# Performance work log

Measured on AMD Instinct MI355X. Metric: run time of the kernel, lower is better.

The kernel has to match this reference:

```python
import jax, jax.numpy as jnp
import numpy as np

B, F, V, D, K = 16384, 39, 30000, 16, 20
EPS = 1e-5


def bn_eval(x, g, b):
    # inference-mode BatchNorm1d with running_mean=0, running_var=1
    return g * x / jnp.sqrt(1.0 + EPS) + b


def setup_inputs() -> dict:
    key = jax.random.key(0)
    ks = jax.random.split(key, 12)
    x = jax.random.randint(ks[0], (B, F), 0, V)
    emb_table = jax.random.normal(ks[1], (F * V, D), dtype=jnp.float32) * 0.05
    w_c = jax.random.normal(ks[2], (F, F * D), dtype=jnp.float32) * 0.05
    w0 = jax.random.normal(ks[3], (1024, F * D), dtype=jnp.float32) * 0.04
    w1 = jax.random.normal(ks[4], (512, 1024), dtype=jnp.float32) * 0.03
    w_out = jax.random.normal(ks[5], (1, 512), dtype=jnp.float32) * 0.04
    return {
        'x': x, 'emb_table': emb_table,
        'w_c': w_c, 'b_c': jnp.zeros((F,)), 'g_c': jnp.ones((F,)), 'be_c': jnp.zeros((F,)),
        'w0': w0, 'b0': jnp.zeros((1024,)), 'g0': jnp.ones((1024,)), 'be0': jnp.zeros((1024,)),
        'w1': w1, 'b1': jnp.zeros((512,)), 'g1': jnp.ones((512,)), 'be1': jnp.zeros((512,)),
        'w_out': w_out, 'b_out': jnp.zeros((1,)),
    }


def reference(x, emb_table, w_c, b_c, g_c, be_c, w0, b0, g0, be0,
              w1, b1, g1, be1, w_out, b_out):
    offsets = jnp.arange(F, dtype=x.dtype) * V          # per-field offsets
    idx = x + offsets[None, :]                          # [B, F]
    emb = emb_table[idx]                                # [B, F, D] gather

    # controller_mlp: flatten (batch, D, F) layout like torch transpose(1,2)
    flat = jnp.transpose(emb, (0, 2, 1)).reshape(B, F * D)
    h = jax.nn.relu(bn_eval(flat @ w_c.T + b_c, g_c, be_c))
    scores = jax.nn.softmax(h, axis=1)                  # [B, F]

    # kmax_pooling: top-k field indices, sorted ascending, gather weights
    _, kidx = jax.lax.top_k(scores, K)
    kidx = jnp.sort(kidx, axis=1)                       # [B, K]
    w = jnp.take_along_axis(scores, kidx, axis=1)       # [B, K]

    # forward_select: gather selected field embeddings, weight them
    sel = jnp.take_along_axis(emb, kidx[:, :, None], axis=1)  # [B, K, D]
    weighted = sel * w[:, :, None]

    # scatter back into full field slots (unselected fields are zero)
    full = jnp.zeros((B, F, D), weighted.dtype)
    bidx = jnp.arange(B)[:, None]
    full = full.at[bidx, kidx].set(weighted)            # [B, F, D]

    z = jnp.transpose(full, (0, 2, 1)).reshape(B, F * D)
    z = jax.nn.relu(bn_eval(z @ w0.T + b0, g0, be0))
    z = jax.nn.relu(bn_eval(z @ w1.T + b1, g1, be1))
    out = jax.nn.sigmoid(z @ w_out.T + b_out)           # [B, 1]
    return out.squeeze(-1)
```

## Files before the change

### kernel.cpp

```cpp
#include <hip/hip_runtime.h>
#include <math.h>

#define B_SZ 16384
#define F_N 39
#define V_N 30000
#define D_N 16
#define K_SEL 20
#define FD 624
#define KP0 640
#define NCP 48
#define N0 1024
#define N1 512
#define CBR 16
#define ALD 648

typedef unsigned short u16;
typedef __attribute__((ext_vector_type(8))) short bf16x8;
typedef __attribute__((ext_vector_type(8))) unsigned short u16x8;
typedef __attribute__((ext_vector_type(4))) float f32x4;

__device__ __forceinline__ float bf2f(u16 v) {
    union { unsigned u; float f; } x; x.u = ((unsigned)v) << 16;
    return x.f;
}
__device__ __forceinline__ unsigned cvtpk2(float a, float b) {
    unsigned d;
    asm("v_cvt_pk_bf16_f32 %0, %1, %2" : "=v"(d) : "v"(a), "v"(b));
    return d;
}

#define GLD16(gp, lp) __builtin_amdgcn_global_load_lds( \
    (const __attribute__((address_space(1))) unsigned int*)(gp), \
    (__attribute__((address_space(3))) unsigned int*)(lp), 16, 0, 0)

#define MFMA16(a, b, c) __builtin_amdgcn_mfma_f32_16x16x32_bf16((a), (b), (c), 0, 0, 0)

__global__ __launch_bounds__(256) void prep_all_kernel(
    const float* __restrict__ w0, const float* __restrict__ w1,
    const float* __restrict__ w_c, const float* __restrict__ b_c,
    const float* __restrict__ g_c, const float* __restrict__ be_c,
    u16* __restrict__ w0b, u16* __restrict__ w1b, u16* __restrict__ wcb,
    float* __restrict__ bcp, float* __restrict__ gcp, float* __restrict__ becp)
{
    __shared__ float Lb[8][624];
    const int bid = blockIdx.x;
    const int t   = threadIdx.x;

    if (bid < 134) {
        const bool is_w0 = (bid < 128);
        const int r0 = is_w0 ? bid * 8 : (bid - 128) * 8;
        const int nrows_src = is_w0 ? N0 : F_N;
        const float* __restrict__ src = is_w0 ? w0 : w_c;
        u16* __restrict__ dst = is_w0 ? w0b : wcb;

        for (int j = t; j < 8 * 156; j += 256) {
            const int row = j / 156;
            const int c4  = j - row * 156;
            const int n   = r0 + row;
            if (n < nrows_src)
                *(float4*)&Lb[row][c4 * 4] =
                    *(const float4*)&src[(size_t)n * FD + c4 * 4];
        }
        __syncthreads();

        for (int j = t; j < 8 * 320; j += 256) {
            const int row = j / 320;
            const int pr  = j - row * 320;
            const int n   = r0 + row;
            const int k0  = pr * 2;
            float v0 = 0.f, v1 = 0.f;
            if (n < nrows_src) {
                const int d0 = k0 & 15,       f0 = k0 >> 4;
                const int d1 = (k0 + 1) & 15, f1 = (k0 + 1) >> 4;
                if (f0 < F_N) v0 = Lb[row][d0 * F_N + f0];
                if (f1 < F_N) v1 = Lb[row][d1 * F_N + f1];
            }
            *(unsigned*)&dst[(size_t)n * KP0 + k0] = cvtpk2(v0, v1);
        }
        return;
    }
    if (bid < 390) {
        const size_t e0 = (size_t)(bid - 134) * 2048 + t * 8;
        float4 v0 = *(const float4*)(w1 + e0);
        float4 v1 = *(const float4*)(w1 + e0 + 4);
        uint4 o = { cvtpk2(v0.x, v0.y), cvtpk2(v0.z, v0.w),
                    cvtpk2(v1.x, v1.y), cvtpk2(v1.z, v1.w) };
        *(uint4*)(w1b + e0) = o;
        return;
    }
    if (t < 3 * NCP) {
        const int which = t / NCP, n = t - which * NCP;
        float v = 0.f;
        if (n < F_N) v = (which == 0) ? b_c[n] : (which == 1) ? g_c[n] : be_c[n];
        ((which == 0) ? bcp : (which == 1) ? gcp : becp)[n] = v;
    }
}

__global__ __launch_bounds__(256) void fused_controller_kernel(
    const int* __restrict__ x, const float* __restrict__ emb_table,
    const u16* __restrict__ wcb, const float* __restrict__ bcp,
    const float* __restrict__ gcp, const float* __restrict__ becp,
    u16* __restrict__ zb)
{
    __shared__ __align__(16) u16 Al[CBR * ALD];
    __shared__ float vv[CBR][49];
    __shared__ f32x4 part[4][64][3];
    __shared__ float selw[CBR][F_N];

    const int t    = threadIdx.x;
    const int wave = t >> 6;
    const int lane = t & 63;
    const int b0   = blockIdx.x * CBR;

    {
        const int p0 = t, p1 = t + 256, p2 = t + 512;
        const int xi0 = x[b0 * F_N + p0];
        const int xi1 = x[b0 * F_N + p1];
        const int xi2 = (p2 < CBR * F_N) ? x[b0 * F_N + p2] : 0;
        const int pp[3] = { p0, p1, p2 };
        const int xx[3] = { xi0, xi1, xi2 };
        #pragma unroll
        for (int s = 0; s < 3; ++s) {
            const int p = pp[s];
            if (p < CBR * F_N) {
                const int row = p / F_N;
                const int f   = p - row * F_N;
                const float4* src =
                    (const float4*)(emb_table + (size_t)(xx[s] + f * V_N) * D_N);
                float4 v0 = src[0], v1 = src[1], v2 = src[2], v3 = src[3];
                uint4 o0 = { cvtpk2(v0.x, v0.y), cvtpk2(v0.z, v0.w),
                             cvtpk2(v1.x, v1.y), cvtpk2(v1.z, v1.w) };
                uint4 o1 = { cvtpk2(v2.x, v2.y), cvtpk2(v2.z, v2.w),
                             cvtpk2(v3.x, v3.y), cvtpk2(v3.z, v3.w) };
                *(uint4*)&Al[row * ALD + f * D_N]     = o0;
                *(uint4*)&Al[row * ALD + f * D_N + 8] = o1;
            }
        }
    }
    __syncthreads();

    const int m = lane & 15;
    const int q = lane >> 4;
    f32x4 acc0 = {}, acc1 = {}, acc2 = {};
    {
        const u16* ap  = &Al[m * ALD + wave * 160 + q * 8];
        const u16* bp0 = wcb + (size_t)(0  + m) * KP0 + wave * 160 + q * 8;
        const u16* bp1 = wcb + (size_t)(16 + m) * KP0 + wave * 160 + q * 8;
        const u16* bp2 = wcb + (size_t)(32 + m) * KP0 + wave * 160 + q * 8;
        #pragma unroll
        for (int k = 0; k < 5; ++k) {
            bf16x8 af = *(const bf16x8*)ap;
            bf16x8 b0r = *(const bf16x8*)bp0;
            bf16x8 b1r = *(const bf16x8*)bp1;
            bf16x8 b2r = *(const bf16x8*)bp2;
            acc0 = MFMA16(af, b0r, acc0);
            acc1 = MFMA16(af, b1r, acc1);
            acc2 = MFMA16(af, b2r, acc2);
            ap += 32; bp0 += 32; bp1 += 32; bp2 += 32;
        }
    }
    part[wave][lane][0] = acc0;
    part[wave][lane][1] = acc1;
    part[wave][lane][2] = acc2;
    __syncthreads();

    {
        f32x4 r0 = part[0][lane][0] + part[1][lane][0] + part[2][lane][0] + part[3][lane][0];
        f32x4 r1 = part[0][lane][1] + part[1][lane][1] + part[2][lane][1] + part[3][lane][1];
        f32x4 r2 = part[0][lane][2] + part[1][lane][2] + part[2][lane][2] + part[3][lane][2];

        const float rs = rsqrtf(1.0f + 1e-5f);
        if (q == wave) {
            #pragma unroll
            for (int j = 0; j < 3; ++j) {
                const f32x4 a = (j == 0) ? r0 : (j == 1) ? r1 : r2;
                const int n = j * 16 + m;
                const float gn = gcp[n] * rs;
                const float bn = becp[n];
                const float bi = bcp[n];
                #pragma unroll
                for (int r = 0; r < 4; ++r)
                    vv[wave * 4 + r][n] = fmaxf(fmaf(gn, a[r] + bi, bn), 0.f);
            }
        }
    }
    __syncthreads();

    {
        const int row = wave * 4 + (lane >> 4);
        const int fl  = lane & 15;
        float e[3] = {0.f, 0.f, 0.f};
        float mloc = -1e30f;
        #pragma unroll
        for (int it = 0; it < 3; ++it) {
            const int f = fl + 16 * it;
            if (f < F_N) { e[it] = vv[row][f]; mloc = fmaxf(mloc, e[it]); }
        }
        mloc = fmaxf(mloc, __shfl_xor(mloc, 1, 64));
        mloc = fmaxf(mloc, __shfl_xor(mloc, 2, 64));
        mloc = fmaxf(mloc, __shfl_xor(mloc, 4, 64));
        mloc = fmaxf(mloc, __shfl_xor(mloc, 8, 64));
        float sloc = 0.f;
        #pragma unroll
        for (int it = 0; it < 3; ++it) {
            const int f = fl + 16 * it;
            if (f < F_N) { e[it] = expf(e[it] - mloc); sloc += e[it]; }
        }
        sloc += __shfl_xor(sloc, 1, 64);
        sloc += __shfl_xor(sloc, 2, 64);
        sloc += __shfl_xor(sloc, 4, 64);
        sloc += __shfl_xor(sloc, 8, 64);
        const float inv = 1.f / sloc;
        #pragma unroll
        for (int it = 0; it < 3; ++it) {
            const int f = fl + 16 * it;
            if (f < F_N) vv[row][f] = e[it];
        }

        int rank[3] = {};
        for (int gg = 0; gg < F_N; ++gg) {
            const float o = vv[row][gg];
            #pragma unroll
            for (int it = 0; it < 3; ++it) {
                const int f = fl + 16 * it;
                if (f < F_N)
                    rank[it] += (o > e[it] || (o == e[it] && gg < f)) ? 1 : 0;
            }
        }
        #pragma unroll
        for (int it = 0; it < 3; ++it) {
            const int f = fl + 16 * it;
            if (f < F_N)
                selw[row][f] = (rank[it] < K_SEL) ? e[it] * inv : 0.f;
        }
    }
    __syncthreads();

    for (int gp = t; gp < CBR * 40; gp += 256) {
        const int row  = gp / 40;
        const int slot = gp - row * 40;
        u16* dst = zb + (size_t)(b0 + row) * KP0 + slot * D_N;
        uint4 o0 = {0u,0u,0u,0u}, o1 = {0u,0u,0u,0u};
        if (slot < F_N) {
            const float w = selw[row][slot];
            u16x8 a0 = *(u16x8*)&Al[row * ALD + slot * D_N];
            u16x8 a1 = *(u16x8*)&Al[row * ALD + slot * D_N + 8];
            o0 = (uint4){ cvtpk2(bf2f(a0[0]) * w, bf2f(a0[1]) * w),
                          cvtpk2(bf2f(a0[2]) * w, bf2f(a0[3]) * w),
                          cvtpk2(bf2f(a0[4]) * w, bf2f(a0[5]) * w),
                          cvtpk2(bf2f(a0[6]) * w, bf2f(a0[7]) * w) };
            o1 = (uint4){ cvtpk2(bf2f(a1[0]) * w, bf2f(a1[1]) * w),
                          cvtpk2(bf2f(a1[2]) * w, bf2f(a1[3]) * w),
                          cvtpk2(bf2f(a1[4]) * w, bf2f(a1[5]) * w),
                          cvtpk2(bf2f(a1[6]) * w, bf2f(a1[7]) * w) };
        }
        *(uint4*)dst       = o0;
        *(uint4*)(dst + 8) = o1;
    }
}

__global__ __launch_bounds__(512) void fused_mlp_kernel(
    const u16* __restrict__ Azb, const u16* __restrict__ W0,
    const u16* __restrict__ W1,
    const float* __restrict__ b0v, const float* __restrict__ g0v,
    const float* __restrict__ be0v,
    const float* __restrict__ b1v, const float* __restrict__ g1v,
    const float* __restrict__ be1v,
    const float* __restrict__ wov, const float* __restrict__ bov,
    float* __restrict__ out)
{
    __shared__ __align__(16) u16 SM[3 * 16384];
    __shared__ __align__(16) u16 H0[64 * 264];
    __shared__ float red[4][64];

    const int t    = threadIdx.x;
    const int lane = t & 63;
    const int wave = t >> 6;
    const int wm = wave >> 2, wn = wave & 3;
    const int q = lane >> 4, lr16 = lane & 15;
    const int brow = blockIdx.x * 64;

    const int srow = t >> 2;
    const int cC   = (t & 3) ^ ((t >> 3) & 3);
    const int dA  = t * 8;
    const int dB0 = 2048 + t * 8;
    const int dB1 = 2048 + (t + 512) * 8;

    const u16* gAz = Azb + (size_t)(brow + srow) * KP0 + cC * 8;

    int aoffA[2], boffA[4], aoffB[2], boffB[8];
    #pragma unroll
    for (int i = 0; i < 2; ++i) {
        const int ra = wm * 32 + i * 16 + lr16;
        aoffA[i] = ra * 32 + ((q ^ ((ra >> 1) & 3)) * 8);
        aoffB[i] = ra * 264 + q * 8;
    }
    #pragma unroll
    for (int j = 0; j < 4; ++j) {
        const int rb = wn * 64 + j * 16 + lr16;
        boffA[j] = 2048 + rb * 32 + ((q ^ ((rb >> 1) & 3)) * 8);
    }
    #pragma unroll
    for (int j = 0; j < 8; ++j) {
        const int rb = wn * 128 + j * 16 + lr16;
        boffB[j] = rb * 32 + ((q ^ ((rb >> 1) & 3)) * 8);
    }

    f32x4 acc1[2][8] = {};
    const float rs = rsqrtf(1.0f + 1e-5f);

    for (int nt = 0; nt < 4; ++nt) {
        f32x4 acc0[2][4] = {};
        const u16* pA  = gAz;
        const u16* pB0 = W0 + (size_t)(nt * 256 + srow)       * KP0 + cC * 8;
        const u16* pB1 = W0 + (size_t)(nt * 256 + srow + 128) * KP0 + cC * 8;

        if (t < 256) GLD16(pA, SM + dA);
        GLD16(pB0, SM + dB0);
        GLD16(pB1, SM + dB1);
        pA += 32; pB0 += 32; pB1 += 32;
        if (t < 256) GLD16(pA, SM + 16384 + dA);
        GLD16(pB0, SM + 16384 + dB0);
        GLD16(pB1, SM + 16384 + dB1);
        pA += 32; pB0 += 32; pB1 += 32;

        int cur = 0, stg = 2;
        for (int it = 0; it < 19; ++it) {
            if (t < 256) { asm volatile("s_waitcnt vmcnt(3)" ::: "memory"); }
            else         { asm volatile("s_waitcnt vmcnt(2)" ::: "memory"); }
            __builtin_amdgcn_s_barrier();
            __builtin_amdgcn_sched_barrier(0);
            const u16* sc = SM + cur * 16384;
            bf16x8 a0 = *(const bf16x8*)(sc + aoffA[0]);
            bf16x8 a1 = *(const bf16x8*)(sc + aoffA[1]);
            bf16x8 f0 = *(const bf16x8*)(sc + boffA[0]);
            bf16x8 f1 = *(const bf16x8*)(sc + boffA[1]);
            bf16x8 f2 = *(const bf16x8*)(sc + boffA[2]);
            bf16x8 f3 = *(const bf16x8*)(sc + boffA[3]);
            if (it + 2 < 20) {
                u16* ss = SM + stg * 16384;
                if (t < 256) GLD16(pA, ss + dA);
                GLD16(pB0, ss + dB0);
                GLD16(pB1, ss + dB1);
                pA += 32; pB0 += 32; pB1 += 32;
            }
            asm volatile("s_waitcnt lgkmcnt(0)" ::: "memory");
            __builtin_amdgcn_sched_barrier(0);
            __builtin_amdgcn_s_setprio(1);
            acc0[0][0] = MFMA16(a0, f0, acc0[0][0]);
            acc0[0][1] = MFMA16(a0, f1, acc0[0][1]);
            acc0[0][2] = MFMA16(a0, f2, acc0[0][2]);
            acc0[0][3] = MFMA16(a0, f3, acc0[0][3]);
            acc0[1][0] = MFMA16(a1, f0, acc0[1][0]);
            acc0[1][1] = MFMA16(a1, f1, acc0[1][1]);
            acc0[1][2] = MFMA16(a1, f2, acc0[1][2]);
            acc0[1][3] = MFMA16(a1, f3, acc0[1][3]);
            __builtin_amdgcn_s_setprio(0);
            cur = (cur == 2) ? 0 : cur + 1;
            stg = (stg == 2) ? 0 : stg + 1;
        }
        asm volatile("s_waitcnt vmcnt(0)" ::: "memory");
        __builtin_amdgcn_s_barrier();
        __builtin_amdgcn_sched_barrier(0);
        {
            const u16* sc = SM + 16384;
            bf16x8 a0 = *(const bf16x8*)(sc + aoffA[0]);
            bf16x8 a1 = *(const bf16x8*)(sc + aoffA[1]);
            bf16x8 f0 = *(const bf16x8*)(sc + boffA[0]);
            bf16x8 f1 = *(const bf16x8*)(sc + boffA[1]);
            bf16x8 f2 = *(const bf16x8*)(sc + boffA[2]);
            bf16x8 f3 = *(const bf16x8*)(sc + boffA[3]);
            asm volatile("s_waitcnt lgkmcnt(0)" ::: "memory");
            __builtin_amdgcn_sched_barrier(0);
            __builtin_amdgcn_s_setprio(1);
            acc0[0][0] = MFMA16(a0, f0, acc0[0][0]);
            acc0[0][1] = MFMA16(a0, f1, acc0[0][1]);
            acc0[0][2] = MFMA16(a0, f2, acc0[0][2]);
            acc0[0][3] = MFMA16(a0, f3, acc0[0][3]);
            acc0[1][0] = MFMA16(a1, f0, acc0[1][0]);
            acc0[1][1] = MFMA16(a1, f1, acc0[1][1]);
            acc0[1][2] = MFMA16(a1, f2, acc0[1][2]);
            acc0[1][3] = MFMA16(a1, f3, acc0[1][3]);
            __builtin_amdgcn_s_setprio(0);
        }

        const u16* pC = W1 + (size_t)srow * N0 + nt * 256 + cC * 8;
        {
            GLD16(pC,               SM + t * 8);
            GLD16(pC + 131072,      SM + (t + 512) * 8);
            GLD16(pC + 262144,      SM + (t + 1024) * 8);
            GLD16(pC + 393216,      SM + (t + 1536) * 8);
            u16* s2 = SM + 2 * 16384;
            GLD16(pC + 32,          s2 + t * 8);
            GLD16(pC + 131072 + 32, s2 + (t + 512) * 8);
            GLD16(pC + 262144 + 32, s2 + (t + 1024) * 8);
            GLD16(pC + 393216 + 32, s2 + (t + 1536) * 8);
        }

        #pragma unroll
        for (int j = 0; j < 4; ++j) {
            const int n = nt * 256 + wn * 64 + j * 16 + lr16;
            const float gg = g0v[n] * rs;
            const float bb = be0v[n];
            const float bi = b0v[n];
            const int colL = wn * 64 + j * 16 + lr16;
            #pragma unroll
            for (int i = 0; i < 2; ++i) {
                const int mlb = wm * 32 + i * 16 + q * 4;
                float v0 = fmaxf(fmaf(gg, acc0[i][j][0] + bi, bb), 0.f);
                float v1 = fmaxf(fmaf(gg, acc0[i][j][1] + bi, bb), 0.f);
                float v2 = fmaxf(fmaf(gg, acc0[i][j][2] + bi, bb), 0.f);
                float v3 = fmaxf(fmaf(gg, acc0[i][j][3] + bi, bb), 0.f);
                unsigned pa = cvtpk2(v0, v1);
                unsigned pb = cvtpk2(v2, v3);
                H0[(mlb + 0) * 264 + colL] = (u16)pa;
                H0[(mlb + 1) * 264 + colL] = (u16)(pa >> 16);
                H0[(mlb + 2) * 264 + colL] = (u16)pb;
                H0[(mlb + 3) * 264 + colL] = (u16)(pb >> 16);
            }
        }
        asm volatile("s_waitcnt lgkmcnt(0)" ::: "memory");
        __builtin_amdgcn_s_barrier();

        const u16* pCk = pC + 64;
        int cb = 0, sb = 1;
        for (int ks = 0; ks < 7; ++ks) {
            asm volatile("s_waitcnt vmcnt(4)" ::: "memory");
            __builtin_amdgcn_s_barrier();
            __builtin_amdgcn_sched_barrier(0);
            const u16* sc = SM + cb * 16384;
            bf16x8 a0 = *(const bf16x8*)(&H0[aoffB[0] + ks * 32]);
            bf16x8 a1 = *(const bf16x8*)(&H0[aoffB[1] + ks * 32]);
            bf16x8 f0 = *(const bf16x8*)(sc + boffB[0]);
            bf16x8 f1 = *(const bf16x8*)(sc + boffB[1]);
            bf16x8 f2 = *(const bf16x8*)(sc + boffB[2]);
            bf16x8 f3 = *(const bf16x8*)(sc + boffB[3]);
            bf16x8 f4 = *(const bf16x8*)(sc + boffB[4]);
            bf16x8 f5 = *(const bf16x8*)(sc + boffB[5]);
            bf16x8 f6 = *(const bf16x8*)(sc + boffB[6]);
            bf16x8 f7 = *(const bf16x8*)(sc + boffB[7]);
            if (ks + 2 < 8) {
                u16* ss = SM + sb * 16384;
                GLD16(pCk,          ss + t * 8);
                GLD16(pCk + 131072, ss + (t + 512) * 8);
                GLD16(pCk + 262144, ss + (t + 1024) * 8);
                GLD16(pCk + 393216, ss + (t + 1536) * 8);
                pCk += 32;
            }
            asm volatile("s_waitcnt lgkmcnt(0)" ::: "memory");
            __builtin_amdgcn_sched_barrier(0);
            __builtin_amdgcn_s_setprio(1);
            acc1[0][0] = MFMA16(a0, f0, acc1[0][0]);
            acc1[0][1] = MFMA16(a0, f1, acc1[0][1]);
            acc1[0][2] = MFMA16(a0, f2, acc1[0][2]);
            acc1[0][3] = MFMA16(a0, f3, acc1[0][3]);
            acc1[0][4] = MFMA16(a0, f4, acc1[0][4]);
            acc1[0][5] = MFMA16(a0, f5, acc1[0][5]);
            acc1[0][6] = MFMA16(a0, f6, acc1[0][6]);
            acc1[0][7] = MFMA16(a0, f7, acc1[0][7]);
            acc1[1][0] = MFMA16(a1, f0, acc1[1][0]);
            acc1[1][1] = MFMA16(a1, f1, acc1[1][1]);
            acc1[1][2] = MFMA16(a1, f2, acc1[1][2]);
            acc1[1][3] = MFMA16(a1, f3, acc1[1][3]);
            acc1[1][4] = MFMA16(a1, f4, acc1[1][4]);
            acc1[1][5] = MFMA16(a1, f5, acc1[1][5]);
            acc1[1][6] = MFMA16(a1, f6, acc1[1][6]);
            acc1[1][7] = MFMA16(a1, f7, acc1[1][7]);
            __builtin_amdgcn_s_setprio(0);
            cb = (cb == 0) ? 2 : cb - 1;
            sb = (sb == 0) ? 2 : sb - 1;
        }
        asm volatile("s_waitcnt vmcnt(0)" ::: "memory");
        __builtin_amdgcn_s_barrier();
        __builtin_amdgcn_sched_barrier(0);
        {
            const u16* sc = SM + 2 * 16384;
            bf16x8 a0 = *(const bf16x8*)(&H0[aoffB[0] + 7 * 32]);
            bf16x8 a1 = *(const bf16x8*)(&H0[aoffB[1] + 7 * 32]);
            bf16x8 f0 = *(const bf16x8*)(sc + boffB[0]);
            bf16x8 f1 = *(const bf16x8*)(sc + boffB[1]);
            bf16x8 f2 = *(const bf16x8*)(sc + boffB[2]);
            bf16x8 f3 = *(const bf16x8*)(sc + boffB[3]);
            bf16x8 f4 = *(const bf16x8*)(sc + boffB[4]);
            bf16x8 f5 = *(const bf16x8*)(sc + boffB[5]);
            bf16x8 f6 = *(const bf16x8*)(sc + boffB[6]);
            bf16x8 f7 = *(const bf16x8*)(sc + boffB[7]);
            asm volatile("s_waitcnt lgkmcnt(0)" ::: "memory");
            __builtin_amdgcn_sched_barrier(0);
            __builtin_amdgcn_s_setprio(1);
            acc1[0][0] = MFMA16(a0, f0, acc1[0][0]);
            acc1[0][1] = MFMA16(a0, f1, acc1[0][1]);
            acc1[0][2] = MFMA16(a0, f2, acc1[0][2]);
            acc1[0][3] = MFMA16(a0, f3, acc1[0][3]);
            acc1[0][4] = MFMA16(a0, f4, acc1[0][4]);
            acc1[0][5] = MFMA16(a0, f5, acc1[0][5]);
            acc1[0][6] = MFMA16(a0, f6, acc1[0][6]);
            acc1[0][7] = MFMA16(a0, f7, acc1[0][7]);
            acc1[1][0] = MFMA16(a1, f0, acc1[1][0]);
            acc1[1][1] = MFMA16(a1, f1, acc1[1][1]);
            acc1[1][2] = MFMA16(a1, f2, acc1[1][2]);
            acc1[1][3] = MFMA16(a1, f3, acc1[1][3]);
            acc1[1][4] = MFMA16(a1, f4, acc1[1][4]);
            acc1[1][5] = MFMA16(a1, f5, acc1[1][5]);
            acc1[1][6] = MFMA16(a1, f6, acc1[1][6]);
            acc1[1][7] = MFMA16(a1, f7, acc1[1][7]);
            __builtin_amdgcn_s_setprio(0);
        }
    }

    float s[2][4] = {};
    #pragma unroll
    for (int j = 0; j < 8; ++j) {
        const int n1 = wn * 128 + j * 16 + lr16;
        const float wv = wov[n1];
        const float gg = g1v[n1] * rs;
        const float bb = be1v[n1];
        const float bi = b1v[n1];
        #pragma unroll
        for (int i = 0; i < 2; ++i)
            #pragma unroll
            for (int r = 0; r < 4; ++r) {
                float v = fmaxf(fmaf(gg, acc1[i][j][r] + bi, bb), 0.f);
                s[i][r] = fmaf(v, wv, s[i][r]);
            }
    }
    #pragma unroll
    for (int i = 0; i < 2; ++i)
        #pragma unroll
        for (int r = 0; r < 4; ++r) {
            float v = s[i][r];
            v += __shfl_xor(v, 1, 64);
            v += __shfl_xor(v, 2, 64);
            v += __shfl_xor(v, 4, 64);
            v += __shfl_xor(v, 8, 64);
            s[i][r] = v;
        }
    if (lr16 == 0) {
        #pragma unroll
        for (int i = 0; i < 2; ++i)
            #pragma unroll
            for (int r = 0; r < 4; ++r)
                red[wn][wm * 32 + i * 16 + q * 4 + r] = s[i][r];
    }
    __syncthreads();
    if (t < 64) {
        const float v = red[0][t] + red[1][t] + red[2][t] + red[3][t] + bov[0];
        out[brow + t] = 1.f / (1.f + expf(-v));
    }
}

extern "C" void kernel_launch(void* const* d_in, const int* in_sizes, int n_in,
                              void* d_out, int out_size, void* d_ws, size_t ws_size,
                              hipStream_t stream)
{
    const int*   x     = (const int*)  d_in[0];
    const float* emb   = (const float*)d_in[1];
    const float* w_c   = (const float*)d_in[2];
    const float* b_c   = (const float*)d_in[3];
    const float* g_c   = (const float*)d_in[4];
    const float* be_c  = (const float*)d_in[5];
    const float* w0    = (const float*)d_in[6];
    const float* b0    = (const float*)d_in[7];
    const float* g0    = (const float*)d_in[8];
    const float* be0   = (const float*)d_in[9];
    const float* w1    = (const float*)d_in[10];
    const float* b1    = (const float*)d_in[11];
    const float* g1    = (const float*)d_in[12];
    const float* be1   = (const float*)d_in[13];
    const float* w_out = (const float*)d_in[14];
    const float* b_out = (const float*)d_in[15];
    float* out = (float*)d_out;

    u16*   zb    = (u16*)d_ws;
    u16*   w0b   = zb  + (size_t)B_SZ * KP0;
    u16*   w1b   = w0b + (size_t)N0 * KP0;
    u16*   wcb   = w1b + (size_t)N1 * N0;
    float* bcp   = (float*)(wcb + (size_t)NCP * KP0);
    float* gcp   = bcp + NCP;
    float* becp  = gcp + NCP;

    prep_all_kernel<<<391, 256, 0, stream>>>(
        w0, w1, w_c, b_c, g_c, be_c, w0b, w1b, wcb, bcp, gcp, becp);

    fused_controller_kernel<<<B_SZ / CBR, 256, 0, stream>>>(
        x, emb, wcb, bcp, gcp, becp, zb);

    fused_mlp_kernel<<<B_SZ / 64, 512, 0, stream>>>(
        zb, w0b, w1b, b0, g0, be0, b1, g1, be1, w_out, b_out, out);
}
```

Measured before the change: 221.8 us.

## Halve fused MLP row tile to 32 and shrink shared memory for occupancy

The fused MLP kernel now processes 32 batch rows per block instead of 64, doubling the grid to 512 blocks. Shared memory shrinks: stage slots are 9216 elements, the hidden-layer buffer is 32x256 with an XOR swizzle, and the second GEMM is split into two halves of 256 output columns that reuse the same staging slots. The aim is more blocks per CU and better latency hiding on the 256-CU device. The cost is that W0 and W1 are re-streamed twice as often across blocks, and each wave issues fewer MFMAs per LDS load.

```diff
diff --git a/kernel.cpp b/kernel.cpp
--- a/kernel.cpp
+++ b/kernel.cpp
@@ -13,6 +13,7 @@
 #define N1 512
 #define CBR 16
 #define ALD 648
+#define SLOT 9216
 
 typedef unsigned short u16;
 typedef __attribute__((ext_vector_type(8))) short bf16x8;
@@ -269,92 +270,75 @@
     const float* __restrict__ wov, const float* __restrict__ bov,
     float* __restrict__ out)
 {
-    __shared__ __align__(16) u16 SM[3 * 16384];
-    __shared__ __align__(16) u16 H0[64 * 264];
-    __shared__ float red[4][64];
+    __shared__ __align__(16) u16 SM[3 * SLOT + 32 * 256];
+    __shared__ float red[4][32];
 
     const int t    = threadIdx.x;
     const int lane = t & 63;
     const int wave = t >> 6;
     const int wm = wave >> 2, wn = wave & 3;
     const int q = lane >> 4, lr16 = lane & 15;
-    const int brow = blockIdx.x * 64;
-
-    const int srow = t >> 2;
-    const int cC   = (t & 3) ^ ((t >> 3) & 3);
-    const int dA  = t * 8;
-    const int dB0 = 2048 + t * 8;
-    const int dB1 = 2048 + (t + 512) * 8;
-
-    const u16* gAz = Azb + (size_t)(brow + srow) * KP0 + cC * 8;
-
-    int aoffA[2], boffA[4], aoffB[2], boffB[8];
-    #pragma unroll
-    for (int i = 0; i < 2; ++i) {
-        const int ra = wm * 32 + i * 16 + lr16;
-        aoffA[i] = ra * 32 + ((q ^ ((ra >> 1) & 3)) * 8);
-        aoffB[i] = ra * 264 + q * 8;
-    }
+    const int brow = blockIdx.x * 32;
+
+    u16* const H0 = SM + 3 * SLOT;
+
+    const int rS = t >> 2;
+    const int cA = (t & 3) ^ ((rS >> 1) & 3);
+
+    const int raA   = wm * 16 + lr16;
+    const int aoffA = raA * 32 + ((q ^ ((raA >> 1) & 3)) * 8);
+    int boff[4];
     #pragma unroll
     for (int j = 0; j < 4; ++j) {
         const int rb = wn * 64 + j * 16 + lr16;
-        boffA[j] = 2048 + rb * 32 + ((q ^ ((rb >> 1) & 3)) * 8);
-    }
-    #pragma unroll
-    for (int j = 0; j < 8; ++j) {
-        const int rb = wn * 128 + j * 16 + lr16;
-        boffB[j] = rb * 32 + ((q ^ ((rb >> 1) & 3)) * 8);
-    }
-
-    f32x4 acc1[2][8] = {};
+        boff[j] = 1024 + rb * 32 + ((q ^ ((rb >> 1) & 3)) * 8);
+    }
+    const int rhB = wm * 16 + lr16;
+
+    f32x4 acc1[2][4] = {};
     const float rs = rsqrtf(1.0f + 1e-5f);
 
     for (int nt = 0; nt < 4; ++nt) {
-        f32x4 acc0[2][4] = {};
-        const u16* pA  = gAz;
-        const u16* pB0 = W0 + (size_t)(nt * 256 + srow)       * KP0 + cC * 8;
-        const u16* pB1 = W0 + (size_t)(nt * 256 + srow + 128) * KP0 + cC * 8;
-
-        if (t < 256) GLD16(pA, SM + dA);
-        GLD16(pB0, SM + dB0);
-        GLD16(pB1, SM + dB1);
+        f32x4 acc0[4] = {};
+        const u16* pA  = Azb + (size_t)(brow + rS) * KP0 + cA * 8;
+        const u16* pB0 = W0 + (size_t)(nt * 256 + rS) * KP0 + cA * 8;
+        const u16* pB1 = pB0 + (size_t)128 * KP0;
+
+        if (t < 128) GLD16(pA, SM + t * 8);
+        GLD16(pB0, SM + 1024 + t * 8);
+        GLD16(pB1, SM + 1024 + (t + 512) * 8);
         pA += 32; pB0 += 32; pB1 += 32;
-        if (t < 256) GLD16(pA, SM + 16384 + dA);
-        GLD16(pB0, SM + 16384 + dB0);
-        GLD16(pB1, SM + 16384 + dB1);
+        if (t < 128) GLD16(pA, SM + SLOT + t * 8);
+        GLD16(pB0, SM + SLOT + 1024 + t * 8);
+        GLD16(pB1, SM + SLOT + 1024 + (t + 512) * 8);
         pA += 32; pB0 += 32; pB1 += 32;
 
         int cur = 0, stg = 2;
         for (int it = 0; it < 19; ++it) {
-            if (t < 256) { asm volatile("s_waitcnt vmcnt(3)" ::: "memory"); }
-            else         { asm volatile("s_waitcnt vmcnt(2)" ::: "memory"); }
+            if (wave < 2) { asm volatile("s_waitcnt vmcnt(3)" ::: "memory"); }
+            else          { asm volatile("s_waitcnt vmcnt(2)" ::: "memory"); }
             __builtin_amdgcn_s_barrier();
             __builtin_amdgcn_sched_barrier(0);
-            const u16* sc = SM + cur * 16384;
-            bf16x8 a0 = *(const bf16x8*)(sc + aoffA[0]);
-            bf16x8 a1 = *(const bf16x8*)(sc + aoffA[1]);
-            bf16x8 f0 = *(const bf16x8*)(sc + boffA[0]);
-            bf16x8 f1 = *(const bf16x8*)(sc + boffA[1]);
-            bf16x8 f2 = *(const bf16x8*)(sc + boffA[2]);
-            bf16x8 f3 = *(const bf16x8*)(sc + boffA[3]);
+            const u16* sc = SM + cur * SLOT;
+            bf16x8 a0 = *(const bf16x8*)(sc + aoffA);
+            bf16x8 f0 = *(const bf16x8*)(sc + boff[0]);
+            bf16x8 f1 = *(const bf16x8*)(sc + boff[1]);
+            bf16x8 f2 = *(const bf16x8*)(sc + boff[2]);
+            bf16x8 f3 = *(const bf16x8*)(sc + boff[3]);
             if (it + 2 < 20) {
-                u16* ss = SM + stg * 16384;
-                if (t < 256) GLD16(pA, ss + dA);
-                GLD16(pB0, ss + dB0);
-                GLD16(pB1, ss + dB1);
+                u16* ss = SM + stg * SLOT;
+                if (t < 128) GLD16(pA, ss + t * 8);
+                GLD16(pB0, ss + 1024 + t * 8);
+                GLD16(pB1, ss + 1024 + (t + 512) * 8);
                 pA += 32; pB0 += 32; pB1 += 32;
             }
             asm volatile("s_waitcnt lgkmcnt(0)" ::: "memory");
             __builtin_amdgcn_sched_barrier(0);
             __builtin_amdgcn_s_setprio(1);
-            acc0[0][0] = MFMA16(a0, f0, acc0[0][0]);
-            acc0[0][1] = MFMA16(a0, f1, acc0[0][1]);
-            acc0[0][2] = MFMA16(a0, f2, acc0[0][2]);
-            acc0[0][3] = MFMA16(a0, f3, acc0[0][3]);
-            acc0[1][0] = MFMA16(a1, f0, acc0[1][0]);
-            acc0[1][1] = MFMA16(a1, f1, acc0[1][1]);
-            acc0[1][2] = MFMA16(a1, f2, acc0[1][2]);
-            acc0[1][3] = MFMA16(a1, f3, acc0[1][3]);
+            acc0[0] = MFMA16(a0, f0, acc0[0]);
+            acc0[1] = MFMA16(a0, f1, acc0[1]);
+            acc0[2] = MFMA16(a0, f2, acc0[2]);
+            acc0[3] = MFMA16(a0, f3, acc0[3]);
             __builtin_amdgcn_s_setprio(0);
             cur = (cur == 2) ? 0 : cur + 1;
             stg = (stg == 2) ? 0 : stg + 1;
@@ -363,39 +347,28 @@
         __builtin_amdgcn_s_barrier();
         __builtin_amdgcn_sched_barrier(0);
         {
-            const u16* sc = SM + 16384;
-            bf16x8 a0 = *(const bf16x8*)(sc + aoffA[0]);
-            bf16x8 a1 = *(const bf16x8*)(sc + aoffA[1]);
-            bf16x8 f0 = *(const bf16x8*)(sc + boffA[0]);
-            bf16x8 f1 = *(const bf16x8*)(sc + boffA[1]);
-            bf16x8 f2 = *(const bf16x8*)(sc + boffA[2]);
-            bf16x8 f3 = *(const bf16x8*)(sc + boffA[3]);
+            const u16* sc = SM + SLOT;
+            bf16x8 a0 = *(const bf16x8*)(sc + aoffA);
+            bf16x8 f0 = *(const bf16x8*)(sc + boff[0]);
+            bf16x8 f1 = *(const bf16x8*)(sc + boff[1]);
+            bf16x8 f2 = *(const bf16x8*)(sc + boff[2]);
+            bf16x8 f3 = *(const bf16x8*)(sc + boff[3]);
             asm volatile("s_waitcnt lgkmcnt(0)" ::: "memory");
             __builtin_amdgcn_sched_barrier(0);
             __builtin_amdgcn_s_setprio(1);
-            acc0[0][0] = MFMA16(a0, f0, acc0[0][0]);
-            acc0[0][1] = MFMA16(a0, f1, acc0[0][1]);
-            acc0[0][2] = MFMA16(a0, f2, acc0[0][2]);
-            acc0[0][3] = MFMA16(a0, f3, acc0[0][3]);
-            acc0[1][0] = MFMA16(a1, f0, acc0[1][0]);
-            acc0[1][1] = MFMA16(a1, f1, acc0[1][1]);
-            acc0[1][2] = MFMA16(a1, f2, acc0[1][2]);
-            acc0[1][3] = MFMA16(a1, f3, acc0[1][3]);
+            acc0[0] = MFMA16(a0, f0, acc0[0]);
+            acc0[1] = MFMA16(a0, f1, acc0[1]);
+            acc0[2] = MFMA16(a0, f2, acc0[2]);
+            acc0[3] = MFMA16(a0, f3, acc0[3]);
             __builtin_amdgcn_s_setprio(0);
         }
-
-        const u16* pC = W1 + (size_t)srow * N0 + nt * 256 + cC * 8;
-        {
-            GLD16(pC,               SM + t * 8);
-            GLD16(pC + 131072,      SM + (t + 512) * 8);
-            GLD16(pC + 262144,      SM + (t + 1024) * 8);
-            GLD16(pC + 393216,      SM + (t + 1536) * 8);
-            u16* s2 = SM + 2 * 16384;
-            GLD16(pC + 32,          s2 + t * 8);
-            GLD16(pC + 131072 + 32, s2 + (t + 512) * 8);
-            GLD16(pC + 262144 + 32, s2 + (t + 1024) * 8);
-            GLD16(pC + 393216 + 32, s2 + (t + 1536) * 8);
-        }
+        __builtin_amdgcn_s_barrier();
+
+        const u16* pC0 = W1 + (size_t)rS * N0 + nt * 256 + cA * 8;
+        GLD16(pC0,          SM + 1024 + t * 8);
+        GLD16(pC0 + 131072, SM + 1024 + (t + 512) * 8);
+        GLD16(pC0 + 32,          SM + SLOT + 1024 + t * 8);
+        GLD16(pC0 + 131072 + 32, SM + SLOT + 1024 + (t + 512) * 8);
 
         #pragma unroll
         for (int j = 0; j < 4; ++j) {
@@ -403,147 +376,119 @@
             const float gg = g0v[n] * rs;
             const float bb = be0v[n];
             const float bi = b0v[n];
-            const int colL = wn * 64 + j * 16 + lr16;
+            const int col = wn * 64 + j * 16 + lr16;
+            float v0 = fmaxf(fmaf(gg, acc0[j][0] + bi, bb), 0.f);
+            float v1 = fmaxf(fmaf(gg, acc0[j][1] + bi, bb), 0.f);
+            float v2 = fmaxf(fmaf(gg, acc0[j][2] + bi, bb), 0.f);
+            float v3 = fmaxf(fmaf(gg, acc0[j][3] + bi, bb), 0.f);
+            unsigned pa = cvtpk2(v0, v1);
+            unsigned pb = cvtpk2(v2, v3);
             #pragma unroll
-            for (int i = 0; i < 2; ++i) {
-                const int mlb = wm * 32 + i * 16 + q * 4;
-                float v0 = fmaxf(fmaf(gg, acc0[i][j][0] + bi, bb), 0.f);
-                float v1 = fmaxf(fmaf(gg, acc0[i][j][1] + bi, bb), 0.f);
-                float v2 = fmaxf(fmaf(gg, acc0[i][j][2] + bi, bb), 0.f);
-                float v3 = fmaxf(fmaf(gg, acc0[i][j][3] + bi, bb), 0.f);
-                unsigned pa = cvtpk2(v0, v1);
-                unsigned pb = cvtpk2(v2, v3);
-                H0[(mlb + 0) * 264 + colL] = (u16)pa;
-                H0[(mlb + 1) * 264 + colL] = (u16)(pa >> 16);
-                H0[(mlb + 2) * 264 + colL] = (u16)pb;
-                H0[(mlb + 3) * 264 + colL] = (u16)(pb >> 16);
+            for (int r = 0; r < 4; ++r) {
+                const int row = wm * 16 + q * 4 + r;
+                const unsigned pk = (r < 2) ? pa : pb;
+                const u16 val = (r & 1) ? (u16)(pk >> 16) : (u16)pk;
+                H0[row * 256 + (((col >> 3) ^ (row & 7)) * 8) + (col & 7)] = val;
             }
         }
         asm volatile("s_waitcnt lgkmcnt(0)" ::: "memory");
         __builtin_amdgcn_s_barrier();
 
-        const u16* pCk = pC + 64;
-        int cb = 0, sb = 1;
-        for (int ks = 0; ks < 7; ++ks) {
-            asm volatile("s_waitcnt vmcnt(4)" ::: "memory");
+        #pragma unroll
+        for (int h = 0; h < 2; ++h) {
+            if (h == 1) {
+                const u16* pCh = W1 + (size_t)(256 + rS) * N0 + nt * 256 + cA * 8;
+                GLD16(pCh,          SM + 1024 + t * 8);
+                GLD16(pCh + 131072, SM + 1024 + (t + 512) * 8);
+                GLD16(pCh + 32,          SM + SLOT + 1024 + t * 8);
+                GLD16(pCh + 131072 + 32, SM + SLOT + 1024 + (t + 512) * 8);
+            }
+            const u16* pCk = W1 + (size_t)(h * 256 + rS) * N0 + nt * 256 + cA * 8 + 64;
+            int cb = 0, sb = 2;
+            for (int ks = 0; ks < 7; ++ks) {
+                asm volatile("s_waitcnt vmcnt(2)" ::: "memory");
+                __builtin_amdgcn_s_barrier();
+                __builtin_amdgcn_sched_barrier(0);
+                const u16* sc = SM + cb * SLOT;
+                const int c8 = ks * 4 + q;
+                bf16x8 a0 = *(const bf16x8*)(&H0[rhB * 256 + ((c8 ^ (rhB & 7)) * 8)]);
+                bf16x8 f0 = *(const bf16x8*)(sc + boff[0]);
+                bf16x8 f1 = *(const bf16x8*)(sc + boff[1]);
+                bf16x8 f2 = *(const bf16x8*)(sc + boff[2]);
+                bf16x8 f3 = *(const bf16x8*)(sc + boff[3]);
+                if (ks + 2 < 8) {
+                    u16* ss = SM + sb * SLOT;
+                    GLD16(pCk,          ss + 1024 + t * 8);
+                    GLD16(pCk + 131072, ss + 1024 + (t + 512) * 8);
+                    pCk += 32;
+                }
+                asm volatile("s_waitcnt lgkmcnt(0)" ::: "memory");
+                __builtin_amdgcn_sched_barrier(0);
+                __builtin_amdgcn_s_setprio(1);
+                acc1[h][0] = MFMA16(a0, f0, acc1[h][0]);
+                acc1[h][1] = MFMA16(a0, f1, acc1[h][1]);
+                acc1[h][2] = MFMA16(a0, f2, acc1[h][2]);
+                acc1[h][3] = MFMA16(a0, f3, acc1[h][3]);
+                __builtin_amdgcn_s_setprio(0);
+                cb = (cb == 2) ? 0 : cb + 1;
+                sb = (sb == 2) ? 0 : sb + 1;
+            }
+            asm volatile("s_waitcnt vmcnt(0)" ::: "memory");
             __builtin_amdgcn_s_barrier();
             __builtin_amdgcn_sched_barrier(0);
-            const u16* sc = SM + cb * 16384;
-            bf16x8 a0 = *(const bf16x8*)(&H0[aoffB[0] + ks * 32]);
-            bf16x8 a1 = *(const bf16x8*)(&H0[aoffB[1] + ks * 32]);
-            bf16x8 f0 = *(const bf16x8*)(sc + boffB[0]);
-            bf16x8 f1 = *(const bf16x8*)(sc + boffB[1]);
-            bf16x8 f2 = *(const bf16x8*)(sc + boffB[2]);
-            bf16x8 f3 = *(const bf16x8*)(sc + boffB[3]);
-            bf16x8 f4 = *(const bf16x8*)(sc + boffB[4]);
-            bf16x8 f5 = *(const bf16x8*)(sc + boffB[5]);
-            bf16x8 f6 = *(const bf16x8*)(sc + boffB[6]);
-            bf16x8 f7 = *(const bf16x8*)(sc + boffB[7]);
-            if (ks + 2 < 8) {
-                u16* ss = SM + sb * 16384;
-                GLD16(pCk,          ss + t * 8);
-                GLD16(pCk + 131072, ss + (t + 512) * 8);
-                GLD16(pCk + 262144, ss + (t + 1024) * 8);
-                GLD16(pCk + 393216, ss + (t + 1536) * 8);
-                pCk += 32;
-            }
-            asm volatile("s_waitcnt lgkmcnt(0)" ::: "memory");
-            __builtin_amdgcn_sched_barrier(0);
-            __builtin_amdgcn_s_setprio(1);
-            acc1[0][0] = MFMA16(a0, f0, acc1[0][0]);
-            acc1[0][1] = MFMA16(a0, f1, acc1[0][1]);
-            acc1[0][2] = MFMA16(a0, f2, acc1[0][2]);
-            acc1[0][3] = MFMA16(a0, f3, acc1[0][3]);
-            acc1[0][4] = MFMA16(a0, f4, acc1[0][4]);
-            acc1[0][5] = MFMA16(a0, f5, acc1[0][5]);
-            acc1[0][6] = MFMA16(a0, f6, acc1[0][6]);
-            acc1[0][7] = MFMA16(a0, f7, acc1[0][7]);
-            acc1[1][0] = MFMA16(a1, f0, acc1[1][0]);
-            acc1[1][1] = MFMA16(a1, f1, acc1[1][1]);
-            acc1[1][2] = MFMA16(a1, f2, acc1[1][2]);
-            acc1[1][3] = MFMA16(a1, f3, acc1[1][3]);
-            acc1[1][4] = MFMA16(a1, f4, acc1[1][4]);
-            acc1[1][5] = MFMA16(a1, f5, acc1[1][5]);
-            acc1[1][6] = MFMA16(a1, f6, acc1[1][6]);
-            acc1[1][7] = MFMA16(a1, f7, acc1[1][7]);
-            __builtin_amdgcn_s_setprio(0);
-            cb = (cb == 0) ? 2 : cb - 1;
-            sb = (sb == 0) ? 2 : sb - 1;
-        }
-        asm volatile("s_waitcnt vmcnt(0)" ::: "memory");
-        __builtin_amdgcn_s_barrier();
-        __builtin_amdgcn_sched_barrier(0);
-        {
-            const u16* sc = SM + 2 * 16384;
-            bf16x8 a0 = *(const bf16x8*)(&H0[aoffB[0] + 7 * 32]);
-            bf16x8 a1 = *(const bf16x8*)(&H0[aoffB[1] + 7 * 32]);
-            bf16x8 f0 = *(const bf16x8*)(sc + boffB[0]);
-            bf16x8 f1 = *(const bf16x8*)(sc + boffB[1]);
-            bf16x8 f2 = *(const bf16x8*)(sc + boffB[2]);
-            bf16x8 f3 = *(const bf16x8*)(sc + boffB[3]);
-            bf16x8 f4 = *(const bf16x8*)(sc + boffB[4]);
-            bf16x8 f5 = *(const bf16x8*)(sc + boffB[5]);
-            bf16x8 f6 = *(const bf16x8*)(sc + boffB[6]);
-            bf16x8 f7 = *(const bf16x8*)(sc + boffB[7]);
-            asm volatile("s_waitcnt lgkmcnt(0)" ::: "memory");
-            __builtin_amdgcn_sched_barrier(0);
-            __builtin_amdgcn_s_setprio(1);
-            acc1[0][0] = MFMA16(a0, f0, acc1[0][0]);
-            acc1[0][1] = MFMA16(a0, f1, acc1[0][1]);
-            acc1[0][2] = MFMA16(a0, f2, acc1[0][2]);
-            acc1[0][3] = MFMA16(a0, f3, acc1[0][3]);
-            acc1[0][4] = MFMA16(a0, f4, acc1[0][4]);
-            acc1[0][5] = MFMA16(a0, f5, acc1[0][5]);
-            acc1[0][6] = MFMA16(a0, f6, acc1[0][6]);
-            acc1[0][7] = MFMA16(a0, f7, acc1[0][7]);
-            acc1[1][0] = MFMA16(a1, f0, acc1[1][0]);
-            acc1[1][1] = MFMA16(a1, f1, acc1[1][1]);
-            acc1[1][2] = MFMA16(a1, f2, acc1[1][2]);
-            acc1[1][3] = MFMA16(a1, f3, acc1[1][3]);
-            acc1[1][4] = MFMA16(a1, f4, acc1[1][4]);
-            acc1[1][5] = MFMA16(a1, f5, acc1[1][5]);
-            acc1[1][6] = MFMA16(a1, f6, acc1[1][6]);
-            acc1[1][7] = MFMA16(a1, f7, acc1[1][7]);
-            __builtin_amdgcn_s_setprio(0);
-        }
-    }
-
-    float s[2][4] = {};
+            {
+                const u16* sc = SM + SLOT;
+                const int c8 = 7 * 4 + q;
+                bf16x8 a0 = *(const bf16x8*)(&H0[rhB * 256 + ((c8 ^ (rhB & 7)) * 8)]);
+                bf16x8 f0 = *(const bf16x8*)(sc + boff[0]);
+                bf16x8 f1 = *(const bf16x8*)(sc + boff[1]);
+                bf16x8 f2 = *(const bf16x8*)(sc + boff[2]);
+                bf16x8 f3 = *(const bf16x8*)(sc + boff[3]);
+                asm volatile("s_waitcnt lgkmcnt(0)" ::: "memory");
+                __builtin_amdgcn_sched_barrier(0);
+                __builtin_amdgcn_s_setprio(1);
+                acc1[h][0] = MFMA16(a0, f0, acc1[h][0]);
+                acc1[h][1] = MFMA16(a0, f1, acc1[h][1]);
+                acc1[h][2] = MFMA16(a0, f2, acc1[h][2]);
+                acc1[h][3] = MFMA16(a0, f3, acc1[h][3]);
+                __builtin_amdgcn_s_setprio(0);
+            }
+            __builtin_amdgcn_s_barrier();
+        }
+    }
+
+    float s[4] = {0.f, 0.f, 0.f, 0.f};
     #pragma unroll
-    for (int j = 0; j < 8; ++j) {
-        const int n1 = wn * 128 + j * 16 + lr16;
-        const float wv = wov[n1];
-        const float gg = g1v[n1] * rs;
-        const float bb = be1v[n1];
-        const float bi = b1v[n1];
-        #pragma unroll
-        for (int i = 0; i < 2; ++i)
+    for (int h = 0; h < 2; ++h)
+        #pragma unroll
+        for (int j = 0; j < 4; ++j) {
+            const int n1 = h * 256 + wn * 64 + j * 16 + lr16;
+            const float wv = wov[n1];
+            const float gg = g1v[n1] * rs;
+            const float bb = be1v[n1];
+            const float bi = b1v[n1];
             #pragma unroll
             for (int r = 0; r < 4; ++r) {
-                float v = fmaxf(fmaf(gg, acc1[i][j][r] + bi, bb), 0.f);
-                s[i][r] = fmaf(v, wv, s[i][r]);
-            }
-    }
+                float v = fmaxf(fmaf(gg, acc1[h][j][r] + bi, bb), 0.f);
+                s[r] = fmaf(v, wv, s[r]);
+            }
+        }
     #pragma unroll
-    for (int i = 0; i < 2; ++i)
-        #pragma unroll
-        for (int r = 0; r < 4; ++r) {
-            float v = s[i][r];
-            v += __shfl_xor(v, 1, 64);
-            v += __shfl_xor(v, 2, 64);
-            v += __shfl_xor(v, 4, 64);
-            v += __shfl_xor(v, 8, 64);
-            s[i][r] = v;
-        }
+    for (int r = 0; r < 4; ++r) {
+        float v = s[r];
+        v += __shfl_xor(v, 1, 64);
+        v += __shfl_xor(v, 2, 64);
+        v += __shfl_xor(v, 4, 64);
+        v += __shfl_xor(v, 8, 64);
+        s[r] = v;
+    }
     if (lr16 == 0) {
         #pragma unroll
-        for (int i = 0; i < 2; ++i)
-            #pragma unroll
-            for (int r = 0; r < 4; ++r)
-                red[wn][wm * 32 + i * 16 + q * 4 + r] = s[i][r];
+        for (int r = 0; r < 4; ++r)
+            red[wn][wm * 16 + q * 4 + r] = s[r];
     }
     __syncthreads();
-    if (t < 64) {
+    if (t < 32) {
         const float v = red[0][t] + red[1][t] + red[2][t] + red[3][t] + bov[0];
         out[brow + t] = 1.f / (1.f + expf(-v));
     }
@@ -585,6 +530,6 @@
     fused_controller_kernel<<<B_SZ / CBR, 256, 0, stream>>>(
         x, emb, wcb, bcp, gcp, becp, zb);
 
-    fused_mlp_kernel<<<B_SZ / 64, 512, 0, stream>>>(
+    fused_mlp_kernel<<<B_SZ / 32, 512, 0, stream>>>(
         zb, w0b, w1b, b0, g0, be0, b1, g1, be1, w_out, b_out, out);
 }
```

Measured after the change: 274.1 us. 23.5% more time.
